# Performance work log

Measured on AMD Instinct MI355X. Metric: run time of the kernel, lower is better.

The kernel has to match this reference:

```python
import jax, jax.numpy as jnp
import numpy as np

ITERATION = 10

def setup_inputs() -> dict:
    key = jax.random.key(0)
    k1, k2, k3 = jax.random.split(key, 3)
    a_inter = jax.random.normal(k1, (8, 64, 64, 32, 32), dtype=jnp.float32)
    logits = jax.random.normal(k2, (8, 64), dtype=jnp.float32)
    W = jax.random.normal(k3, (1, 64, 64), dtype=jnp.float32)
    return {"a_inter": a_inter, "logits": logits, "W": W}


def reference(a_inter, logits, W):
    N = W.shape[1]  # num_nodes
    B = a_inter.shape[0]
    # feats: [B, N, C*H*W]
    feats = a_inter[:, :, :N, :, :].reshape(B, N, -1)
    # expand logits [B, N] -> [B, N, N] (unsqueeze(1).expand in torch)
    logits0 = jnp.broadcast_to(logits[:, None, :], (B, N, N))

    feats_norm = jnp.linalg.norm(feats, ord=2, axis=2, keepdims=True)  # [B, N, 1]
    pairwise_norm = feats_norm @ jnp.swapaxes(feats_norm, 1, 2)        # [B, N, N]
    pairwise_dot = feats @ jnp.swapaxes(feats, 1, 2)                   # [B, N, N]
    pairwise_sim = pairwise_dot / (pairwise_norm + 1e-6)
    W_sym = (W + jnp.swapaxes(W, 1, 2)) / 2.0
    pairwise_potential = pairwise_sim * W_sym                          # [B, N, N]

    unary_potential = logits0

    def body(i, l):
        probs = jnp.swapaxes(jax.nn.sigmoid(l), 1, 2)  # [B, N, N]
        # probs*pp - (1-probs)*pp == (2*probs - 1)*pp
        pp_E = jnp.sum((2.0 * probs - 1.0) * pairwise_potential, axis=2, keepdims=True)
        return unary_potential + pp_E

    logits_out = jax.lax.fori_loop(0, ITERATION, body, logits0)
    return logits_out.mean(axis=1)  # [B, N]
```

## Files before the change

### kernel.cpp

```cpp
#include <hip/hip_runtime.h>
#include <math.h>

#define BATCH 8
#define NN 64
#define DD 65536
#define CH 128
#define KC (DD / CH)
#define KSTEPS (KC / 32)

typedef float  floatx4 __attribute__((ext_vector_type(4)));
typedef __bf16 bf16x8  __attribute__((ext_vector_type(8)));

static __device__ __forceinline__ bf16x8 cvt8(float4 lo, float4 hi) {
    const unsigned sel = 0x07060302u;
    union { unsigned u[4]; bf16x8 v; } r;
    r.u[0] = __builtin_amdgcn_perm(__float_as_uint(lo.y), __float_as_uint(lo.x), sel);
    r.u[1] = __builtin_amdgcn_perm(__float_as_uint(lo.w), __float_as_uint(lo.z), sel);
    r.u[2] = __builtin_amdgcn_perm(__float_as_uint(hi.y), __float_as_uint(hi.x), sel);
    r.u[3] = __builtin_amdgcn_perm(__float_as_uint(hi.w), __float_as_uint(hi.z), sel);
    return r.v;
}

__global__ __launch_bounds__(256, 4) void gram_partial_kernel(const float* __restrict__ a,
                                                              float* __restrict__ part) {
    const int bid = blockIdx.x;
    const int b = bid >> 7;
    const int c = bid & (CH - 1);

    const int tid  = threadIdx.x;
    const int w    = tid >> 6;
    const int lane = tid & 63;
    const int m    = lane & 15;
    const int q    = lane >> 4;

    const float* base = a + (size_t)b * NN * DD + (size_t)c * KC
                          + (size_t)m * DD + q * 8;
    const float* p[4];
    #pragma unroll
    for (int i = 0; i < 4; ++i)
        p[i] = base + (size_t)((w ^ i) * 16) * DD;

    floatx4 acc[4];
    #pragma unroll
    for (int i = 0; i < 4; ++i) acc[i] = (floatx4)0.0f;

    #pragma unroll
    for (int s = 0; s < KSTEPS; ++s) {
        const int o = s * 32;
        float4 l0 = *(const float4*)(p[0] + o);
        float4 h0 = *(const float4*)(p[0] + o + 4);
        float4 l1 = *(const float4*)(p[1] + o);
        float4 h1 = *(const float4*)(p[1] + o + 4);
        float4 l2 = *(const float4*)(p[2] + o);
        float4 h2 = *(const float4*)(p[2] + o + 4);
        float4 l3 = *(const float4*)(p[3] + o);
        float4 h3 = *(const float4*)(p[3] + o + 4);

        bf16x8 f0 = cvt8(l0, h0);
        bf16x8 f1 = cvt8(l1, h1);
        bf16x8 f2 = cvt8(l2, h2);
        bf16x8 f3 = cvt8(l3, h3);

        acc[0] = __builtin_amdgcn_mfma_f32_16x16x32_bf16(f0, f0, acc[0], 0, 0, 0);
        acc[1] = __builtin_amdgcn_mfma_f32_16x16x32_bf16(f0, f1, acc[1], 0, 0, 0);
        acc[2] = __builtin_amdgcn_mfma_f32_16x16x32_bf16(f0, f2, acc[2], 0, 0, 0);
        acc[3] = __builtin_amdgcn_mfma_f32_16x16x32_bf16(f0, f3, acc[3], 0, 0, 0);
    }

    float* pg = part + (size_t)bid * (NN * NN);
    #pragma unroll
    for (int i = 0; i < 4; ++i) {
        const int t = w ^ i;
        float* tp = pg + (w * 4 + t) * 256 + m;
        #pragma unroll
        for (int r = 0; r < 4; ++r)
            tp[(q * 4 + r) * 16] = acc[i][r];
    }
}

__global__ __launch_bounds__(128) void gram_reduce_kernel(const float* __restrict__ part,
                                                          float* __restrict__ gram) {
    const int gid = blockIdx.x * 128 + threadIdx.x;
    const int b   = gid >> 12;
    const int idx = gid & 4095;
    const int i   = idx >> 6;
    const int j   = idx & 63;
    const int off = ((i >> 4) * 4 + (j >> 4)) * 256 + (i & 15) * 16 + (j & 15);
    const float* p = part + (size_t)b * CH * (NN * NN) + off;

    float s0 = 0.f, s1 = 0.f, s2 = 0.f, s3 = 0.f;
    #pragma unroll
    for (int c = 0; c < CH; c += 4) {
        s0 += p[(size_t)(c + 0) * (NN * NN)];
        s1 += p[(size_t)(c + 1) * (NN * NN)];
        s2 += p[(size_t)(c + 2) * (NN * NN)];
        s3 += p[(size_t)(c + 3) * (NN * NN)];
    }
    gram[gid] = (s0 + s1) + (s2 + s3);
}

__global__ __launch_bounds__(256) void crf_kernel(const float* __restrict__ gram,
                                                  const float* __restrict__ logits,
                                                  const float* __restrict__ Wm,
                                                  float* __restrict__ out) {
    __shared__ float pp[NN][NN + 1];
    __shared__ float E[NN];
    __shared__ float nrm[NN];
    __shared__ float part[4 * NN];

    const int b  = blockIdx.x;
    const int tid = threadIdx.x;
    const int i  = tid & 63;
    const int jq = tid >> 6;
    const float* g = gram + b * NN * NN;

    if (jq == 0) nrm[i] = sqrtf(g[i * NN + i]);
    E[i] = 0.0f;
    __syncthreads();

    const float ni = nrm[i];
    for (int jj = 0; jj < 16; ++jj) {
        int j = jq * 16 + jj;
        float wsym = 0.5f * (Wm[i * NN + j] + Wm[j * NN + i]);
        pp[i][j] = g[i * NN + j] / (ni * nrm[j] + 1e-6f) * wsym;
    }
    const float li = logits[b * NN + i];
    __syncthreads();

    for (int it = 0; it < 10; ++it) {
        float acc = 0.0f;
        for (int jj = 0; jj < 16; ++jj) {
            int j = jq * 16 + jj;
            float t = li + E[j];
            float s = 1.0f / (1.0f + expf(-t));
            acc = fmaf(2.0f * s - 1.0f, pp[i][j], acc);
        }
        part[jq * NN + i] = acc;
        __syncthreads();
        if (jq == 0)
            E[i] = part[i] + part[NN + i] + part[2 * NN + i] + part[3 * NN + i];
        __syncthreads();
    }

    if (tid < 64) {
        float s = E[tid];
        for (int off = 32; off > 0; off >>= 1) s += __shfl_down(s, off);
        float meanE = __shfl(s, 0) * (1.0f / 64.0f);
        out[b * NN + tid] = logits[b * NN + tid] + meanE;
    }
}

extern "C" void kernel_launch(void* const* d_in, const int* in_sizes, int n_in,
                              void* d_out, int out_size, void* d_ws, size_t ws_size,
                              hipStream_t stream) {
    const float* a      = (const float*)d_in[0];
    const float* logits = (const float*)d_in[1];
    const float* Wm     = (const float*)d_in[2];
    float* out  = (float*)d_out;

    float* part = (float*)d_ws;
    float* gram = part + (size_t)BATCH * CH * NN * NN;

    gram_partial_kernel<<<BATCH * CH, 256, 0, stream>>>(a, part);
    gram_reduce_kernel<<<(BATCH * NN * NN) / 128, 128, 0, stream>>>(part, gram);
    crf_kernel<<<BATCH, 256, 0, stream>>>(gram, logits, Wm, out);
}
```

Measured before the change: 236.4 us.

## Double the gram split count and double-buffer loads ahead of MFMA

Raises the number of K-chunks per batch from 128 to 256, so the partial Gram kernel launches twice as many blocks with half the work each. Its inner loop becomes a register ping-pong: the next step's eight float4 loads are issued before the current step's bf16 convert and MFMA work, to hide global-load latency. The cost is twice the partial-sum workspace and a reduce kernel that reads twice as much data; its unroll is now capped at 4.

```diff
diff --git a/kernel.cpp b/kernel.cpp
--- a/kernel.cpp
+++ b/kernel.cpp
@@ -4,7 +4,7 @@
 #define BATCH 8
 #define NN 64
 #define DD 65536
-#define CH 128
+#define CH 256
 #define KC (DD / CH)
 #define KSTEPS (KC / 32)
 
@@ -24,7 +24,7 @@
 __global__ __launch_bounds__(256, 4) void gram_partial_kernel(const float* __restrict__ a,
                                                               float* __restrict__ part) {
     const int bid = blockIdx.x;
-    const int b = bid >> 7;
+    const int b = bid >> 8;
     const int c = bid & (CH - 1);
 
     const int tid  = threadIdx.x;
@@ -35,37 +35,46 @@
 
     const float* base = a + (size_t)b * NN * DD + (size_t)c * KC
                           + (size_t)m * DD + q * 8;
-    const float* p[4];
-    #pragma unroll
-    for (int i = 0; i < 4; ++i)
-        p[i] = base + (size_t)((w ^ i) * 16) * DD;
+    const float* p0 = base + (size_t)((w ^ 0) * 16) * DD;
+    const float* p1 = base + (size_t)((w ^ 1) * 16) * DD;
+    const float* p2 = base + (size_t)((w ^ 2) * 16) * DD;
+    const float* p3 = base + (size_t)((w ^ 3) * 16) * DD;
 
     floatx4 acc[4];
     #pragma unroll
     for (int i = 0; i < 4; ++i) acc[i] = (floatx4)0.0f;
 
+    float4 A0, A1, A2, A3, A4, A5, A6, A7;
+    float4 B0, B1, B2, B3, B4, B5, B6, B7;
+
+#define LOADSET(R0,R1,R2,R3,R4,R5,R6,R7, o)                      \
+    R0 = *(const float4*)(p0 + (o));  R1 = *(const float4*)(p0 + (o) + 4); \
+    R2 = *(const float4*)(p1 + (o));  R3 = *(const float4*)(p1 + (o) + 4); \
+    R4 = *(const float4*)(p2 + (o));  R5 = *(const float4*)(p2 + (o) + 4); \
+    R6 = *(const float4*)(p3 + (o));  R7 = *(const float4*)(p3 + (o) + 4);
+
+#define MFMASET(R0,R1,R2,R3,R4,R5,R6,R7)                         \
+    {                                                            \
+        bf16x8 f0 = cvt8(R0, R1);                                \
+        bf16x8 f1 = cvt8(R2, R3);                                \
+        bf16x8 f2 = cvt8(R4, R5);                                \
+        bf16x8 f3 = cvt8(R6, R7);                                \
+        acc[0] = __builtin_amdgcn_mfma_f32_16x16x32_bf16(f0, f0, acc[0], 0, 0, 0); \
+        acc[1] = __builtin_amdgcn_mfma_f32_16x16x32_bf16(f0, f1, acc[1], 0, 0, 0); \
+        acc[2] = __builtin_amdgcn_mfma_f32_16x16x32_bf16(f0, f2, acc[2], 0, 0, 0); \
+        acc[3] = __builtin_amdgcn_mfma_f32_16x16x32_bf16(f0, f3, acc[3], 0, 0, 0); \
+    }
+
+    LOADSET(A0,A1,A2,A3,A4,A5,A6,A7, 0)
     #pragma unroll
-    for (int s = 0; s < KSTEPS; ++s) {
-        const int o = s * 32;
-        float4 l0 = *(const float4*)(p[0] + o);
-        float4 h0 = *(const float4*)(p[0] + o + 4);
-        float4 l1 = *(const float4*)(p[1] + o);
-        float4 h1 = *(const float4*)(p[1] + o + 4);
-        float4 l2 = *(const float4*)(p[2] + o);
-        float4 h2 = *(const float4*)(p[2] + o + 4);
-        float4 l3 = *(const float4*)(p[3] + o);
-        float4 h3 = *(const float4*)(p[3] + o + 4);
-
-        bf16x8 f0 = cvt8(l0, h0);
-        bf16x8 f1 = cvt8(l1, h1);
-        bf16x8 f2 = cvt8(l2, h2);
-        bf16x8 f3 = cvt8(l3, h3);
-
-        acc[0] = __builtin_amdgcn_mfma_f32_16x16x32_bf16(f0, f0, acc[0], 0, 0, 0);
-        acc[1] = __builtin_amdgcn_mfma_f32_16x16x32_bf16(f0, f1, acc[1], 0, 0, 0);
-        acc[2] = __builtin_amdgcn_mfma_f32_16x16x32_bf16(f0, f2, acc[2], 0, 0, 0);
-        acc[3] = __builtin_amdgcn_mfma_f32_16x16x32_bf16(f0, f3, acc[3], 0, 0, 0);
+    for (int s = 0; s < KSTEPS; s += 2) {
+        if (s + 1 < KSTEPS) { LOADSET(B0,B1,B2,B3,B4,B5,B6,B7, (s + 1) * 32) }
+        MFMASET(A0,A1,A2,A3,A4,A5,A6,A7)
+        if (s + 2 < KSTEPS) { LOADSET(A0,A1,A2,A3,A4,A5,A6,A7, (s + 2) * 32) }
+        if (s + 1 < KSTEPS) { MFMASET(B0,B1,B2,B3,B4,B5,B6,B7) }
     }
+#undef LOADSET
+#undef MFMASET
 
     float* pg = part + (size_t)bid * (NN * NN);
     #pragma unroll
@@ -89,7 +98,7 @@
     const float* p = part + (size_t)b * CH * (NN * NN) + off;
 
     float s0 = 0.f, s1 = 0.f, s2 = 0.f, s3 = 0.f;
-    #pragma unroll
+    #pragma unroll 4
     for (int c = 0; c < CH; c += 4) {
         s0 += p[(size_t)(c + 0) * (NN * NN)];
         s1 += p[(size_t)(c + 1) * (NN * NN)];
```

After: 251.8 us. +6.5%, slower.
